# Kernel tuning notes

Hardware: AMD Instinct MI355X
Metric: run time of the kernel (lower is better)

## Reference

```python
import jax, jax.numpy as jnp
import numpy as np

EPS_LN = 1e-3
EPS_ATTN = 1e-8
D = 256       # slot_dim == feature_dim (required by the torch code)
H_MLP = 512
NUM_ITERS = 3  # step == 0 -> num_initial_iterations
SCALE = D ** (-0.5)


def _layernorm(x, g, b):
    m = jnp.mean(x, axis=-1, keepdims=True)
    v = jnp.mean(jnp.square(x - m), axis=-1, keepdims=True)
    return (x - m) * jax.lax.rsqrt(v + EPS_LN) * g + b


def _gru_cell(x, h, W_ih, b_ih, W_hh, b_hh):
    # torch GRUCell: W_ih [3D, D], W_hh [3D, D], gate order r, z, n
    gi = x @ W_ih.T + b_ih
    gh = h @ W_hh.T + b_hh
    i_r, i_z, i_n = jnp.split(gi, 3, axis=-1)
    h_r, h_z, h_n = jnp.split(gh, 3, axis=-1)
    r = jax.nn.sigmoid(i_r + h_r)
    z = jax.nn.sigmoid(i_z + h_z)
    n = jnp.tanh(i_n + r * h_n)
    return (1.0 - z) * n + z * h


def setup_inputs() -> dict:
    key = jax.random.key(0)
    ks = jax.random.split(key, 16)
    s = 0.02
    inp = {
        "inputs": jax.random.normal(ks[0], (32, 4096, D), jnp.float32),
        "slots": jax.random.normal(ks[1], (32, 8, D), jnp.float32),
        "step": 0,
        "ln_in_g": jnp.ones((D,), jnp.float32),
        "ln_in_b": jnp.zeros((D,), jnp.float32),
        "ln_slot_g": jnp.ones((D,), jnp.float32),
        "ln_slot_b": jnp.zeros((D,), jnp.float32),
        "ln_mlp_g": jnp.ones((D,), jnp.float32),
        "ln_mlp_b": jnp.zeros((D,), jnp.float32),
        "Wq": jax.random.normal(ks[2], (D, D), jnp.float32) * s,
        "bq": jnp.zeros((D,), jnp.float32),
        "Wk": jax.random.normal(ks[3], (D, D), jnp.float32) * s,
        "bk": jnp.zeros((D,), jnp.float32),
        "Wv": jax.random.normal(ks[4], (D, D), jnp.float32) * s,
        "bv": jnp.zeros((D,), jnp.float32),
        "W_ih": jax.random.normal(ks[5], (3 * D, D), jnp.float32) * s,
        "b_ih": jnp.zeros((3 * D,), jnp.float32),
        "W_hh": jax.random.normal(ks[6], (3 * D, D), jnp.float32) * s,
        "b_hh": jnp.zeros((3 * D,), jnp.float32),
        "W1": jax.random.normal(ks[7], (H_MLP, D), jnp.float32) * s,
        "b1": jnp.zeros((H_MLP,), jnp.float32),
        "W2": jax.random.normal(ks[8], (D, H_MLP), jnp.float32) * s,
        "b2": jnp.zeros((D,), jnp.float32),
    }
    return inp


def reference(inputs, slots, step, ln_in_g, ln_in_b, ln_slot_g, ln_slot_b,
              ln_mlp_g, ln_mlp_b, Wq, bq, Wk, bk, Wv, bv,
              W_ih, b_ih, W_hh, b_hh, W1, b1, W2, b2):
    B = inputs.shape[0]
    x = _layernorm(inputs, ln_in_g, ln_in_b)          # [B, N, D]
    k = x @ Wk.T + bk                                  # [B, N, D]
    v = x @ Wv.T + bv                                  # [B, N, D]
    num_iters = NUM_ITERS  # step == 0 -> num_initial_iterations
    for _ in range(num_iters):
        slots_prev = slots
        s_n = _layernorm(slots, ln_slot_g, ln_slot_b)  # [B, S, D]
        q = s_n @ Wq.T + bq                            # [B, S, D]
        dots = jnp.einsum('bid,bjd->bij', q, k) * SCALE  # [B, S, N]
        attn = jax.nn.softmax(dots, axis=1) + EPS_ATTN   # competitive over slots
        attn = attn / jnp.sum(attn, axis=-1, keepdims=True)
        updates = jnp.einsum('bij,bjd->bid', attn, v)  # [B, S, D]
        slots = _gru_cell(updates.reshape(-1, D), slots_prev.reshape(-1, D),
                          W_ih, b_ih, W_hh, b_hh).reshape(B, -1, D)
        mlp = jax.nn.relu(_layernorm(slots, ln_mlp_g, ln_mlp_b) @ W1.T + b1) @ W2.T + b2
        slots = slots + mlp
    return slots
```

## Files before the change

kernel.cpp:

```cpp
#include <hip/hip_runtime.h>
#include <stdint.h>


typedef __attribute__((ext_vector_type(8))) short bf16x8;
typedef __attribute__((ext_vector_type(4))) float f32x4;

__device__ __forceinline__ float bf2f_lo(uint32_t u) {
    union { uint32_t u; float f; } v; v.u = u << 16; return v.f;
}
__device__ __forceinline__ float bf2f_hi(uint32_t u) {
    union { uint32_t u; float f; } v; v.u = u & 0xffff0000u; return v.f;
}
__device__ __forceinline__ unsigned short f2bf(float f) {
    union { float f; uint32_t u; } v; v.f = f;
    return (unsigned short)((v.u + 0x7fffu + ((v.u >> 16) & 1u)) >> 16);
}
__device__ __forceinline__ void unpack8(uint4 v, float* f) {
    f[0] = bf2f_lo(v.x); f[1] = bf2f_hi(v.x); f[2] = bf2f_lo(v.y); f[3] = bf2f_hi(v.y);
    f[4] = bf2f_lo(v.z); f[5] = bf2f_hi(v.z); f[6] = bf2f_lo(v.w); f[7] = bf2f_hi(v.w);
}
__device__ __forceinline__ float sigf(float x) { return 1.0f / (1.0f + __expf(-x)); }
__device__ __forceinline__ void gld_lds16(const void* g, void* l) {
    __builtin_amdgcn_global_load_lds(
        (__attribute__((address_space(1))) unsigned int*)g,
        (__attribute__((address_space(3))) unsigned int*)l, 16, 0, 0);
}

__global__ __launch_bounds__(256) void prep_k(
    const float* __restrict__ in, const float* __restrict__ ln_in_g,
    const float* __restrict__ ln_in_b, unsigned short* __restrict__ xbf,
    const float* __restrict__ Wk, const float* __restrict__ Wv,
    const float* __restrict__ W_ih, const float* __restrict__ W_hh,
    const float* __restrict__ W1, const float* __restrict__ W2,
    const float* __restrict__ bk, const float* __restrict__ bv,
    const float* __restrict__ b_ih, const float* __restrict__ b_hh,
    unsigned short* __restrict__ Wkv, unsigned short* __restrict__ Wg,
    unsigned short* __restrict__ W1b, unsigned short* __restrict__ W2b,
    float* __restrict__ bkv, float* __restrict__ bg,
    const float* __restrict__ slots_in, const float* __restrict__ g_slot,
    const float* __restrict__ b_slot, const float* __restrict__ Wq,
    const float* __restrict__ bq, unsigned short* __restrict__ qbuf) {
    __shared__ __align__(16) unsigned short A1[8 * 264];
    int bid = blockIdx.x, t = threadIdx.x;
    int wave = t >> 6, lane = t & 63;

    if (bid < 32768) {
        size_t row = (size_t)bid * 4 + wave;
        const float4 x = *(const float4*)(in + row * 256 + lane * 4);
        float s  = x.x + x.y + x.z + x.w;
        float sq = x.x * x.x + x.y * x.y + x.z * x.z + x.w * x.w;
#pragma unroll
        for (int off = 32; off > 0; off >>= 1) {
            s  += __shfl_xor(s,  off, 64);
            sq += __shfl_xor(sq, off, 64);
        }
        float mean = s * (1.0f / 256.0f);
        float rstd = rsqrtf(sq * (1.0f / 256.0f) - mean * mean + 1e-3f);
        float4 g4 = *(const float4*)(ln_in_g + lane * 4);
        float4 b4 = *(const float4*)(ln_in_b + lane * 4);
        uint2 o;
        o.x = (uint32_t)f2bf((x.x - mean) * rstd * g4.x + b4.x) |
              ((uint32_t)f2bf((x.y - mean) * rstd * g4.y + b4.y) << 16);
        o.y = (uint32_t)f2bf((x.z - mean) * rstd * g4.z + b4.z) |
              ((uint32_t)f2bf((x.w - mean) * rstd * g4.w + b4.w) << 16);
        int dst = (((lane >> 1) ^ ((int)row & 7)) << 3) + (lane & 1) * 4;
        *(uint2*)(xbf + row * 256 + dst) = o;
        return;
    }
    if (bid < 36096) {
        int i = (bid - 32768) * 256 + t;
        if (i < 131072) {
            float v = (i < 65536) ? Wk[i] : Wv[i - 65536];
            int col = i >> 8, k = i & 255;
            int dk = ((((k >> 3) ^ (col & 7)) << 3) | (k & 7));
            Wkv[col * 256 + dk] = f2bf(v);
        } else if (i < 524288) {
            int j = i - 131072;
            Wg[j] = f2bf(j < 196608 ? W_ih[j] : W_hh[j - 196608]);
        } else if (i < 655360) W1b[i - 524288] = f2bf(W1[i - 524288]);
        else                   W2b[i - 655360] = f2bf(W2[i - 655360]);
        if (i < 512)           bkv[i] = (i < 256 ? bk[i] : bv[i - 256]);
        else if (i < 2048)   { int j = i - 512; bg[j] = (j < 768 ? b_ih[j] : b_hh[j - 768]); }
        return;
    }
    int b = bid - 36096;
    {
        float4 g4 = *(const float4*)(g_slot + lane * 4);
        float4 b4 = *(const float4*)(b_slot + lane * 4);
#pragma unroll
        for (int rep = 0; rep < 2; ++rep) {
            int s = wave * 2 + rep;
            float4 x = *(const float4*)(slots_in + (size_t)b * 2048 + s * 256 + lane * 4);
            float sm = x.x + x.y + x.z + x.w;
            float sq = x.x * x.x + x.y * x.y + x.z * x.z + x.w * x.w;
#pragma unroll
            for (int off = 32; off > 0; off >>= 1) {
                sm += __shfl_xor(sm, off, 64);
                sq += __shfl_xor(sq, off, 64);
            }
            float mean = sm * (1.0f / 256.0f);
            float rstd = rsqrtf(sq * (1.0f / 256.0f) - mean * mean + 1e-3f);
            uint2 o;
            o.x = (uint32_t)f2bf((x.x - mean) * rstd * g4.x + b4.x) |
                  ((uint32_t)f2bf((x.y - mean) * rstd * g4.y + b4.y) << 16);
            o.y = (uint32_t)f2bf((x.z - mean) * rstd * g4.z + b4.z) |
                  ((uint32_t)f2bf((x.w - mean) * rstd * g4.w + b4.w) << 16);
            *(uint2*)&A1[s * 264 + lane * 4] = o;
        }
    }
    __syncthreads();
    {
        bf16x8 af[8];
#pragma unroll
        for (int ks = 0; ks < 8; ++ks)
            af[ks] = *(const bf16x8*)&A1[(lane & 15) * 264 + ks * 32 + (lane >> 4) * 8];
#pragma unroll
        for (int nt = 0; nt < 4; ++nt) {
            int n0 = (wave * 4 + nt) * 16;
            f32x4 a = {0.f, 0.f, 0.f, 0.f};
#pragma unroll
            for (int ks = 0; ks < 8; ++ks) {
                const float* wp = Wq + (size_t)(n0 + (lane & 15)) * 256 +
                                  ks * 32 + (lane >> 4) * 8;
                float4 wa = *(const float4*)wp;
                float4 wb = *(const float4*)(wp + 4);
                bf16x8 bfr;
                bfr[0] = (short)f2bf(wa.x); bfr[1] = (short)f2bf(wa.y);
                bfr[2] = (short)f2bf(wa.z); bfr[3] = (short)f2bf(wa.w);
                bfr[4] = (short)f2bf(wb.x); bfr[5] = (short)f2bf(wb.y);
                bfr[6] = (short)f2bf(wb.z); bfr[7] = (short)f2bf(wb.w);
                a = __builtin_amdgcn_mfma_f32_16x16x32_bf16(af[ks], bfr, a, 0, 0, 0);
            }
            int col = n0 + (lane & 15);
            float bs = bq[col];
#pragma unroll
            for (int r = 0; r < 4; ++r) {
                int row = (lane >> 4) * 4 + r;
                if (row < 8)
                    qbuf[((size_t)b * 8 + row) * 256 + col] = f2bf(a[r] + bs);
            }
        }
    }
}

__global__ __launch_bounds__(256) void gemm_kv(const unsigned short* __restrict__ X,
                                               const unsigned short* __restrict__ W,
                                               const float* __restrict__ bkv,
                                               unsigned short* __restrict__ Ko,
                                               unsigned short* __restrict__ Vo) {
    __shared__ __align__(16) unsigned short As[128 * 64];
    __shared__ __align__(16) unsigned short Bs[128 * 64];
    int t = threadIdx.x, wave = t >> 6, lane = t & 63;
    int wr = wave >> 1, wc = wave & 1;
    int bid = blockIdx.x;
    int m0 = (((bid >> 5) << 3) | (bid & 7)) * 128;
    int j0 = ((bid >> 3) & 3) * 128;

    f32x4 acc[4][4];
#pragma unroll
    for (int i = 0; i < 4; ++i)
#pragma unroll
        for (int j = 0; j < 4; ++j)
#pragma unroll
            for (int r = 0; r < 4; ++r) acc[i][j][r] = 0.f;

    for (int kb = 0; kb < 4; ++kb) {
        int k0 = kb * 64;
#pragma unroll
        for (int i = 0; i < 4; ++i) {
            int rbase = wave * 32 + i * 8;
            gld_lds16(X + (size_t)(m0 + rbase + (lane >> 3)) * 256 + k0 + (lane & 7) * 8,
                      &As[rbase * 64]);
            gld_lds16(W + (size_t)(j0 + rbase + (lane >> 3)) * 256 + k0 + (lane & 7) * 8,
                      &Bs[rbase * 64]);
        }
        __syncthreads();
#pragma unroll
        for (int kk = 0; kk < 64; kk += 32) {
            int koff = kk + (lane >> 4) * 8;
            int cl = koff >> 3;
            bf16x8 af[4], bf[4];
#pragma unroll
            for (int ti = 0; ti < 4; ++ti) {
                int r = wr * 64 + ti * 16 + (lane & 15);
                af[ti] = *(const bf16x8*)&As[r * 64 + ((cl ^ (r & 7)) << 3)];
            }
#pragma unroll
            for (int tj = 0; tj < 4; ++tj) {
                int c = wc * 64 + tj * 16 + (lane & 15);
                bf[tj] = *(const bf16x8*)&Bs[c * 64 + ((cl ^ (c & 7)) << 3)];
            }
#pragma unroll
            for (int ti = 0; ti < 4; ++ti)
#pragma unroll
                for (int tj = 0; tj < 4; ++tj)
                    acc[ti][tj] = __builtin_amdgcn_mfma_f32_16x16x32_bf16(
                        af[ti], bf[tj], acc[ti][tj], 0, 0, 0);
        }
        __syncthreads();
    }
    bool isK = (j0 < 256);
    unsigned short* base = isK ? Ko : Vo;
#pragma unroll
    for (int ti = 0; ti < 4; ++ti)
#pragma unroll
        for (int tj = 0; tj < 4; ++tj) {
            int col = j0 + wc * 64 + tj * 16 + (lane & 15);
            float bias = bkv[col];
            int outc = col & 255;
#pragma unroll
            for (int r = 0; r < 4; ++r) {
                int row = m0 + wr * 64 + ti * 16 + (lane >> 4) * 4 + r;
                base[(size_t)row * 256 + outc] = f2bf(acc[ti][tj][r] + bias);
            }
        }
}

__global__ __launch_bounds__(256) void attn_fused(
    const unsigned short* __restrict__ qb, const unsigned short* __restrict__ K,
    const unsigned short* __restrict__ V,
    float* __restrict__ upd_p,
    float* __restrict__ sums_p) {
    __shared__ __align__(16) unsigned short qs[8 * 256];
    __shared__ __align__(16) float atf[8 * 256];
    __shared__ __align__(16) float pr[4][8 * 256];
    __shared__ float ssum[8];
    int b = blockIdx.x, ch = blockIdx.y, t = threadIdx.x;
    int wave = t >> 6, lane = t & 63;

    *(uint4*)&qs[t * 8] = ((const uint4*)(qb + b * 2048))[t];
    if (t < 8) ssum[t] = 0.f;
    __syncthreads();

    int sg = t >> 7, np = t & 127;
    int nbase = ch * 256 + np * 2;
    const unsigned short* kr = K + ((size_t)b * 4096 + nbase) * 256;
    float acc[4][2];
#pragma unroll
    for (int i = 0; i < 4; ++i) { acc[i][0] = 0.f; acc[i][1] = 0.f; }
    for (int c = 0; c < 32; ++c) {
        float qf[4][8];
#pragma unroll
        for (int si = 0; si < 4; ++si)
            unpack8(*(const uint4*)&qs[(sg * 4 + si) * 256 + c * 8], qf[si]);
#pragma unroll
        for (int r = 0; r < 2; ++r) {
            float kf[8];
            unpack8(*(const uint4*)(kr + (size_t)r * 256 + c * 8), kf);
#pragma unroll
            for (int si = 0; si < 4; ++si)
                acc[si][r] += qf[si][0] * kf[0] + qf[si][1] * kf[1] +
                              qf[si][2] * kf[2] + qf[si][3] * kf[3] +
                              qf[si][4] * kf[4] + qf[si][5] * kf[5] +
                              qf[si][6] * kf[6] + qf[si][7] * kf[7];
        }
    }
#pragma unroll
    for (int si = 0; si < 4; ++si) {
        atf[(sg * 4 + si) * 256 + np * 2 + 0] = acc[si][0] * 0.0625f;
        atf[(sg * 4 + si) * 256 + np * 2 + 1] = acc[si][1] * 0.0625f;
    }
    __syncthreads();

    {
        int n = t;
        float v[8];
#pragma unroll
        for (int s = 0; s < 8; ++s) v[s] = atf[s * 256 + n];
        float m = v[0];
#pragma unroll
        for (int s = 1; s < 8; ++s) m = fmaxf(m, v[s]);
        float sum = 0.f;
#pragma unroll
        for (int s = 0; s < 8; ++s) { v[s] = __expf(v[s] - m); sum += v[s]; }
        float inv = 1.0f / sum;
        float ts[8];
#pragma unroll
        for (int s = 0; s < 8; ++s) {
            float a = v[s] * inv + 1e-8f;
            atf[s * 256 + n] = a;
            ts[s] = a;
        }
#pragma unroll
        for (int s = 0; s < 8; ++s) {
#pragma unroll
            for (int off = 32; off > 0; off >>= 1)
                ts[s] += __shfl_xor(ts[s], off, 64);
        }
        if (lane == 0) {
#pragma unroll
            for (int s = 0; s < 8; ++s) atomicAdd(&ssum[s], ts[s]);
        }
    }
    __syncthreads();
    if (t < 8) sums_p[ch * 256 + b * 8 + t] = ssum[t];

    float ua[8][4];
#pragma unroll
    for (int s = 0; s < 8; ++s)
#pragma unroll
        for (int k = 0; k < 4; ++k) ua[s][k] = 0.f;
    const unsigned short* vb = V + ((size_t)b * 4096 + ch * 256 + wave * 64) * 256 + lane * 4;
    for (int g = 0; g < 16; ++g) {
        int nl = wave * 64 + g * 4;
        float4 a4[8];
#pragma unroll
        for (int s = 0; s < 8; ++s) a4[s] = *(const float4*)&atf[s * 256 + nl];
        const unsigned short* vrow = vb + (size_t)g * 4 * 256;
#define UPD_STEP(kk, comp)                                                     \
        {                                                                      \
            uint2 vv = *(const uint2*)(vrow + (size_t)kk * 256);               \
            float v0 = bf2f_lo(vv.x), v1 = bf2f_hi(vv.x);                      \
            float v2 = bf2f_lo(vv.y), v3 = bf2f_hi(vv.y);                      \
            _Pragma("unroll")                                                  \
            for (int s = 0; s < 8; ++s) {                                      \
                float a = a4[s].comp;                                          \
                ua[s][0] += a * v0; ua[s][1] += a * v1;                        \
                ua[s][2] += a * v2; ua[s][3] += a * v3;                        \
            }                                                                  \
        }
        UPD_STEP(0, x) UPD_STEP(1, y) UPD_STEP(2, z) UPD_STEP(3, w)
#undef UPD_STEP
    }
#pragma unroll
    for (int s = 0; s < 8; ++s)
        *(float4*)&pr[wave][s * 256 + lane * 4] = *(float4*)ua[s];
    __syncthreads();
    for (int i = t; i < 2048; i += 256)
        upd_p[(size_t)ch * 65536 + (size_t)b * 2048 + i] =
            pr[0][i] + pr[1][i] + pr[2][i] + pr[3][i];
}

__global__ __launch_bounds__(256) void slot_tail(
    const float* __restrict__ upd_p, const float* __restrict__ sums_p,
    const float* __restrict__ cur,
    const unsigned short* __restrict__ Wg, const float* __restrict__ bg,
    const float* __restrict__ g_mlp, const float* __restrict__ b_mlp,
    const unsigned short* __restrict__ W1b, const float* __restrict__ b1,
    const unsigned short* __restrict__ W2b, const float* __restrict__ b2,
    const float* __restrict__ g_slot, const float* __restrict__ b_slot,
    const unsigned short* __restrict__ Wqb, const float* __restrict__ bq,
    float* __restrict__ slots_out, unsigned short* __restrict__ qbuf,
    int do_q) {
    __shared__ float gts[8 * 1536];
    __shared__ float hn[2048];
    __shared__ float sn[2048];
    __shared__ __align__(16) unsigned short A1u[8 * 264];
    __shared__ __align__(16) unsigned short A1h[8 * 264];
    __shared__ __align__(16) unsigned short A1[8 * 264];
    __shared__ __align__(16) unsigned short A2[8 * 520];
    __shared__ float ssum8[8];
    int b = blockIdx.x, t = threadIdx.x;
    int wave = t >> 6, lane = t & 63;

    if (t < 8) {
        float s = 0.f;
#pragma unroll
        for (int c = 0; c < 16; ++c) s += sums_p[c * 256 + b * 8 + t];
        ssum8[t] = s;
    }
    __syncthreads();
    for (int idx = t; idx < 2048; idx += 256) {
        int row = idx >> 8, d = idx & 255;
        float us = 0.f;
#pragma unroll
        for (int c = 0; c < 16; ++c) us += upd_p[(size_t)c * 65536 + b * 2048 + idx];
        A1u[row * 264 + d] = f2bf(us / ssum8[row]);
        A1h[row * 264 + d] = f2bf(cur[(size_t)b * 2048 + idx]);
    }
    __syncthreads();

    {
        const unsigned short* Af = (wave < 2) ? A1u : A1h;
        bf16x8 af[8];
#pragma unroll
        for (int ks = 0; ks < 8; ++ks)
            af[ks] = *(const bf16x8*)&Af[(lane & 15) * 264 + ks * 32 + (lane >> 4) * 8];
#pragma unroll
        for (int nt = 0; nt < 24; ++nt) {
            int n0 = wave * 384 + nt * 16;
            f32x4 a = {0.f, 0.f, 0.f, 0.f};
#pragma unroll
            for (int ks = 0; ks < 8; ++ks) {
                bf16x8 bfr = *(const bf16x8*)(Wg + (size_t)(n0 + (lane & 15)) * 256 +
                                              ks * 32 + (lane >> 4) * 8);
                a = __builtin_amdgcn_mfma_f32_16x16x32_bf16(af[ks], bfr, a, 0, 0, 0);
            }
            int col = n0 + (lane & 15);
            float bs = bg[col];
#pragma unroll
            for (int r = 0; r < 4; ++r) {
                int row = (lane >> 4) * 4 + r;
                if (row < 8) gts[row * 1536 + col] = a[r] + bs;
            }
        }
    }
    __syncthreads();

#pragma unroll
    for (int p = 0; p < 8; ++p) {
        int idx = p * 256 + t;
        int s = idx >> 8, j = idx & 255;
        const float* gr = &gts[s * 1536];
        float r  = sigf(gr[j] + gr[768 + j]);
        float z  = sigf(gr[256 + j] + gr[1024 + j]);
        float nn = tanhf(gr[512 + j] + r * gr[1280 + j]);
        float h  = cur[(size_t)b * 2048 + idx];
        hn[idx] = (1.0f - z) * nn + z * h;
    }
    __syncthreads();

    {
        float4 g4 = *(const float4*)(g_mlp + lane * 4);
        float4 b4 = *(const float4*)(b_mlp + lane * 4);
#pragma unroll
        for (int rep = 0; rep < 2; ++rep) {
            int s = wave * 2 + rep;
            float4 x = *(const float4*)&hn[s * 256 + lane * 4];
            float sm = x.x + x.y + x.z + x.w;
            float sq = x.x * x.x + x.y * x.y + x.z * x.z + x.w * x.w;
#pragma unroll
            for (int off = 32; off > 0; off >>= 1) {
                sm += __shfl_xor(sm, off, 64);
                sq += __shfl_xor(sq, off, 64);
            }
            float mean = sm * (1.0f / 256.0f);
            float rstd = rsqrtf(sq * (1.0f / 256.0f) - mean * mean + 1e-3f);
            uint2 o;
            o.x = (uint32_t)f2bf((x.x - mean) * rstd * g4.x + b4.x) |
                  ((uint32_t)f2bf((x.y - mean) * rstd * g4.y + b4.y) << 16);
            o.y = (uint32_t)f2bf((x.z - mean) * rstd * g4.z + b4.z) |
                  ((uint32_t)f2bf((x.w - mean) * rstd * g4.w + b4.w) << 16);
            *(uint2*)&A1[s * 264 + lane * 4] = o;
        }
    }
    __syncthreads();

    {
        bf16x8 af[8];
#pragma unroll
        for (int ks = 0; ks < 8; ++ks)
            af[ks] = *(const bf16x8*)&A1[(lane & 15) * 264 + ks * 32 + (lane >> 4) * 8];
#pragma unroll
        for (int nt = 0; nt < 8; ++nt) {
            int n0 = (wave * 8 + nt) * 16;
            f32x4 a = {0.f, 0.f, 0.f, 0.f};
#pragma unroll
            for (int ks = 0; ks < 8; ++ks) {
                bf16x8 bfr = *(const bf16x8*)(W1b + (size_t)(n0 + (lane & 15)) * 256 +
                                              ks * 32 + (lane >> 4) * 8);
                a = __builtin_amdgcn_mfma_f32_16x16x32_bf16(af[ks], bfr, a, 0, 0, 0);
            }
            int col = n0 + (lane & 15);
            float bs = b1[col];
#pragma unroll
            for (int r = 0; r < 4; ++r) {
                int row = (lane >> 4) * 4 + r;
                if (row < 8) A2[row * 520 + col] = f2bf(fmaxf(a[r] + bs, 0.f));
            }
        }
    }
    __syncthreads();

    {
        bf16x8 af[16];
#pragma unroll
        for (int ks = 0; ks < 16; ++ks)
            af[ks] = *(const bf16x8*)&A2[(lane & 15) * 520 + ks * 32 + (lane >> 4) * 8];
#pragma unroll
        for (int nt = 0; nt < 4; ++nt) {
            int n0 = (wave * 4 + nt) * 16;
            f32x4 a = {0.f, 0.f, 0.f, 0.f};
#pragma unroll
            for (int ks = 0; ks < 16; ++ks) {
                bf16x8 bfr = *(const bf16x8*)(W2b + (size_t)(n0 + (lane & 15)) * 512 +
                                              ks * 32 + (lane >> 4) * 8);
                a = __builtin_amdgcn_mfma_f32_16x16x32_bf16(af[ks], bfr, a, 0, 0, 0);
            }
            int col = n0 + (lane & 15);
            float bs = b2[col];
#pragma unroll
            for (int r = 0; r < 4; ++r) {
                int row = (lane >> 4) * 4 + r;
                if (row < 8) {
                    float v = a[r] + bs + hn[row * 256 + col];
                    sn[row * 256 + col] = v;
                    slots_out[((size_t)b * 8 + row) * 256 + col] = v;
                }
            }
        }
    }
    if (!do_q) return;
    __syncthreads();

    {
        float4 g4 = *(const float4*)(g_slot + lane * 4);
        float4 b4 = *(const float4*)(b_slot + lane * 4);
#pragma unroll
        for (int rep = 0; rep < 2; ++rep) {
            int s = wave * 2 + rep;
            float4 x = *(const float4*)&sn[s * 256 + lane * 4];
            float sm = x.x + x.y + x.z + x.w;
            float sq = x.x * x.x + x.y * x.y + x.z * x.z + x.w * x.w;
#pragma unroll
            for (int off = 32; off > 0; off >>= 1) {
                sm += __shfl_xor(sm, off, 64);
                sq += __shfl_xor(sq, off, 64);
            }
            float mean = sm * (1.0f / 256.0f);
            float rstd = rsqrtf(sq * (1.0f / 256.0f) - mean * mean + 1e-3f);
            uint2 o;
            o.x = (uint32_t)f2bf((x.x - mean) * rstd * g4.x + b4.x) |
                  ((uint32_t)f2bf((x.y - mean) * rstd * g4.y + b4.y) << 16);
            o.y = (uint32_t)f2bf((x.z - mean) * rstd * g4.z + b4.z) |
                  ((uint32_t)f2bf((x.w - mean) * rstd * g4.w + b4.w) << 16);
            *(uint2*)&A1[s * 264 + lane * 4] = o;
        }
    }
    __syncthreads();

    {
        bf16x8 af[8];
#pragma unroll
        for (int ks = 0; ks < 8; ++ks)
            af[ks] = *(const bf16x8*)&A1[(lane & 15) * 264 + ks * 32 + (lane >> 4) * 8];
#pragma unroll
        for (int nt = 0; nt < 4; ++nt) {
            int n0 = (wave * 4 + nt) * 16;
            f32x4 a = {0.f, 0.f, 0.f, 0.f};
#pragma unroll
            for (int ks = 0; ks < 8; ++ks) {
                bf16x8 bfr = *(const bf16x8*)(Wqb + (size_t)(n0 + (lane & 15)) * 256 +
                                              ks * 32 + (lane >> 4) * 8);
                a = __builtin_amdgcn_mfma_f32_16x16x32_bf16(af[ks], bfr, a, 0, 0, 0);
            }
            int col = n0 + (lane & 15);
            float bs = bq[col];
#pragma unroll
            for (int r = 0; r < 4; ++r) {
                int row = (lane >> 4) * 4 + r;
                if (row < 8)
                    qbuf[((size_t)b * 8 + row) * 256 + col] = f2bf(a[r] + bs);
            }
        }
    }
}

extern "C" void kernel_launch(void* const* d_in, const int* in_sizes, int n_in,
                              void* d_out, int out_size, void* d_ws, size_t ws_size,
                              hipStream_t stream) {
    const float* inputs    = (const float*)d_in[0];
    const float* slots_in  = (const float*)d_in[1];
    const float* ln_in_g   = (const float*)d_in[3];
    const float* ln_in_b   = (const float*)d_in[4];
    const float* ln_slot_g = (const float*)d_in[5];
    const float* ln_slot_b = (const float*)d_in[6];
    const float* ln_mlp_g  = (const float*)d_in[7];
    const float* ln_mlp_b  = (const float*)d_in[8];
    const float* Wq   = (const float*)d_in[9];
    const float* bq   = (const float*)d_in[10];
    const float* Wk   = (const float*)d_in[11];
    const float* bk   = (const float*)d_in[12];
    const float* Wv   = (const float*)d_in[13];
    const float* bv   = (const float*)d_in[14];
    const float* W_ih = (const float*)d_in[15];
    const float* b_ih = (const float*)d_in[16];
    const float* W_hh = (const float*)d_in[17];
    const float* b_hh = (const float*)d_in[18];
    const float* W1   = (const float*)d_in[19];
    const float* b1   = (const float*)d_in[20];
    const float* W2   = (const float*)d_in[21];
    const float* b2   = (const float*)d_in[22];

    char* p = (char*)d_ws;
    size_t off = 0;
    auto take = [&](size_t bytes) -> char* {
        char* r = p + off;
        off += (bytes + 255) & ~(size_t)255;
        return r;
    };
    unsigned short* xbf  = (unsigned short*)take((size_t)131072 * 256 * 2);
    unsigned short* Kb   = (unsigned short*)take((size_t)131072 * 256 * 2);
    unsigned short* Vb   = (unsigned short*)take((size_t)131072 * 256 * 2);
    unsigned short* Wkv  = (unsigned short*)take(131072 * 2);
    unsigned short* Wg   = (unsigned short*)take(393216 * 2);
    unsigned short* W1b  = (unsigned short*)take(131072 * 2);
    unsigned short* W2b  = (unsigned short*)take(131072 * 2);
    unsigned short* Wqb  = (unsigned short*)take(65536 * 2);
    float* bkv   = (float*)take(512 * 4);
    float* bg    = (float*)take(1536 * 4);
    unsigned short* qbuf = (unsigned short*)take(65536 * 2);
    float* upd_p = (float*)take((size_t)16 * 65536 * 4);
    float* sums_p= (float*)take(16 * 256 * 4);
    float* sA    = (float*)take(65536 * 4);
    float* sB    = (float*)take(65536 * 4);


    prep_k<<<36128, 256, 0, stream>>>(inputs, ln_in_g, ln_in_b, xbf,
                                      Wk, Wv, W_ih, W_hh, W1, W2,
                                      bk, bv, b_ih, b_hh,
                                      Wkv, Wg, W1b, W2b, bkv, bg,
                                      slots_in, ln_slot_g, ln_slot_b, Wq, bq, qbuf);
    {
        struct L { static __global__ void k(const float* __restrict__ Wq,
                                            unsigned short* __restrict__ Wqb) {
            int i = blockIdx.x * 256 + threadIdx.x;
            Wqb[i] = f2bf(Wq[i]);
        } };
        L::k<<<256, 256, 0, stream>>>(Wq, Wqb);
    }
    gemm_kv<<<4096, 256, 0, stream>>>(xbf, Wkv, bkv, Kb, Vb);

    const float* cur = slots_in;
    float* nxt[3] = {sA, sB, (float*)d_out};
    for (int it = 0; it < 3; ++it) {
        attn_fused<<<dim3(32, 16), 256, 0, stream>>>(qbuf, Kb, Vb, upd_p, sums_p);
        slot_tail<<<32, 256, 0, stream>>>(upd_p, sums_p, cur, Wg, bg,
                                          ln_mlp_g, ln_mlp_b, W1b, b1, W2b, b2,
                                          ln_slot_g, ln_slot_b, Wqb, bq,
                                          nxt[it], qbuf, it < 2 ? 1 : 0);
        cur = nxt[it];
    }
    (void)in_sizes; (void)n_in; (void)out_size; (void)ws_size;
}
```

Before: 618.2 us.

## Accumulate attention partials with atomics and widen slot_tail to 512 threads

```diff
diff --git a/kernel.cpp b/kernel.cpp
--- a/kernel.cpp
+++ b/kernel.cpp
@@ -39,36 +39,52 @@
     float* __restrict__ bkv, float* __restrict__ bg,
     const float* __restrict__ slots_in, const float* __restrict__ g_slot,
     const float* __restrict__ b_slot, const float* __restrict__ Wq,
-    const float* __restrict__ bq, unsigned short* __restrict__ qbuf) {
+    const float* __restrict__ bq, unsigned short* __restrict__ qbuf,
+    float* __restrict__ upd) {
     __shared__ __align__(16) unsigned short A1[8 * 264];
     int bid = blockIdx.x, t = threadIdx.x;
     int wave = t >> 6, lane = t & 63;
 
-    if (bid < 32768) {
-        size_t row = (size_t)bid * 4 + wave;
-        const float4 x = *(const float4*)(in + row * 256 + lane * 4);
-        float s  = x.x + x.y + x.z + x.w;
-        float sq = x.x * x.x + x.y * x.y + x.z * x.z + x.w * x.w;
+    if (bid < 8192) {
+        size_t rb = (size_t)bid * 16 + wave * 4;
+        const float* rp = in + rb * 256 + lane * 4;
+        float4 x0 = *(const float4*)(rp);
+        float4 x1 = *(const float4*)(rp + 256);
+        float4 x2 = *(const float4*)(rp + 512);
+        float4 x3 = *(const float4*)(rp + 768);
+        float s0 = x0.x + x0.y + x0.z + x0.w, q0 = x0.x*x0.x + x0.y*x0.y + x0.z*x0.z + x0.w*x0.w;
+        float s1 = x1.x + x1.y + x1.z + x1.w, q1 = x1.x*x1.x + x1.y*x1.y + x1.z*x1.z + x1.w*x1.w;
+        float s2 = x2.x + x2.y + x2.z + x2.w, q2 = x2.x*x2.x + x2.y*x2.y + x2.z*x2.z + x2.w*x2.w;
+        float s3 = x3.x + x3.y + x3.z + x3.w, q3 = x3.x*x3.x + x3.y*x3.y + x3.z*x3.z + x3.w*x3.w;
 #pragma unroll
         for (int off = 32; off > 0; off >>= 1) {
-            s  += __shfl_xor(s,  off, 64);
-            sq += __shfl_xor(sq, off, 64);
-        }
-        float mean = s * (1.0f / 256.0f);
-        float rstd = rsqrtf(sq * (1.0f / 256.0f) - mean * mean + 1e-3f);
+            s0 += __shfl_xor(s0, off, 64);  q0 += __shfl_xor(q0, off, 64);
+            s1 += __shfl_xor(s1, off, 64);  q1 += __shfl_xor(q1, off, 64);
+            s2 += __shfl_xor(s2, off, 64);  q2 += __shfl_xor(q2, off, 64);
+            s3 += __shfl_xor(s3, off, 64);  q3 += __shfl_xor(q3, off, 64);
+        }
         float4 g4 = *(const float4*)(ln_in_g + lane * 4);
         float4 b4 = *(const float4*)(ln_in_b + lane * 4);
-        uint2 o;
-        o.x = (uint32_t)f2bf((x.x - mean) * rstd * g4.x + b4.x) |
-              ((uint32_t)f2bf((x.y - mean) * rstd * g4.y + b4.y) << 16);
-        o.y = (uint32_t)f2bf((x.z - mean) * rstd * g4.z + b4.z) |
-              ((uint32_t)f2bf((x.w - mean) * rstd * g4.w + b4.w) << 16);
-        int dst = (((lane >> 1) ^ ((int)row & 7)) << 3) + (lane & 1) * 4;
-        *(uint2*)(xbf + row * 256 + dst) = o;
+        float4 xs[4] = {x0, x1, x2, x3};
+        float ss[4] = {s0, s1, s2, s3}, qq[4] = {q0, q1, q2, q3};
+#pragma unroll
+        for (int i = 0; i < 4; ++i) {
+            float mean = ss[i] * (1.0f / 256.0f);
+            float rstd = rsqrtf(qq[i] * (1.0f / 256.0f) - mean * mean + 1e-3f);
+            float4 x = xs[i];
+            uint2 o;
+            o.x = (uint32_t)f2bf((x.x - mean) * rstd * g4.x + b4.x) |
+                  ((uint32_t)f2bf((x.y - mean) * rstd * g4.y + b4.y) << 16);
+            o.y = (uint32_t)f2bf((x.z - mean) * rstd * g4.z + b4.z) |
+                  ((uint32_t)f2bf((x.w - mean) * rstd * g4.w + b4.w) << 16);
+            size_t row = rb + i;
+            int dst = (((lane >> 1) ^ ((int)row & 7)) << 3) + (lane & 1) * 4;
+            *(uint2*)(xbf + row * 256 + dst) = o;
+        }
         return;
     }
-    if (bid < 36096) {
-        int i = (bid - 32768) * 256 + t;
+    if (bid < 11520) {
+        int i = (bid - 8192) * 256 + t;
         if (i < 131072) {
             float v = (i < 65536) ? Wk[i] : Wv[i - 65536];
             int col = i >> 8, k = i & 255;
@@ -83,7 +99,12 @@
         else if (i < 2048)   { int j = i - 512; bg[j] = (j < 768 ? b_ih[j] : b_hh[j - 768]); }
         return;
     }
-    int b = bid - 36096;
+    if (bid >= 11552) {
+        int i = (bid - 11552) * 1024 + t * 4;
+        if (i < 65792) *(float4*)(upd + i) = make_float4(0.f, 0.f, 0.f, 0.f);
+        return;
+    }
+    int b = bid - 11520;
     {
         float4 g4 = *(const float4*)(g_slot + lane * 4);
         float4 b4 = *(const float4*)(b_slot + lane * 4);
@@ -219,8 +240,7 @@
 __global__ __launch_bounds__(256) void attn_fused(
     const unsigned short* __restrict__ qb, const unsigned short* __restrict__ K,
     const unsigned short* __restrict__ V,
-    float* __restrict__ upd_p,
-    float* __restrict__ sums_p) {
+    float* __restrict__ upd, float* __restrict__ sums) {
     __shared__ __align__(16) unsigned short qs[8 * 256];
     __shared__ __align__(16) float atf[8 * 256];
     __shared__ __align__(16) float pr[4][8 * 256];
@@ -293,7 +313,7 @@
         }
     }
     __syncthreads();
-    if (t < 8) sums_p[ch * 256 + b * 8 + t] = ssum[t];
+    if (t < 8) atomicAdd(&sums[b * 8 + t], ssum[t]);
 
     float ua[8][4];
 #pragma unroll
@@ -326,13 +346,15 @@
     for (int s = 0; s < 8; ++s)
         *(float4*)&pr[wave][s * 256 + lane * 4] = *(float4*)ua[s];
     __syncthreads();
-    for (int i = t; i < 2048; i += 256)
-        upd_p[(size_t)ch * 65536 + (size_t)b * 2048 + i] =
-            pr[0][i] + pr[1][i] + pr[2][i] + pr[3][i];
-}
-
-__global__ __launch_bounds__(256) void slot_tail(
-    const float* __restrict__ upd_p, const float* __restrict__ sums_p,
+    for (int i = t; i < 2048; i += 256) {
+        float vsum = pr[0][i] + pr[1][i] + pr[2][i] + pr[3][i];
+        atomicAdd(&upd[(size_t)b * 2048 + i], vsum);
+    }
+}
+
+__global__ __launch_bounds__(512, 1) void slot_tail(
+    const float* __restrict__ upd, const float* __restrict__ sums,
+    float* __restrict__ upd_w, float* __restrict__ sums_w,
     const float* __restrict__ cur,
     const unsigned short* __restrict__ Wg, const float* __restrict__ bg,
     const float* __restrict__ g_mlp, const float* __restrict__ b_mlp,
@@ -353,32 +375,26 @@
     int b = blockIdx.x, t = threadIdx.x;
     int wave = t >> 6, lane = t & 63;
 
-    if (t < 8) {
-        float s = 0.f;
-#pragma unroll
-        for (int c = 0; c < 16; ++c) s += sums_p[c * 256 + b * 8 + t];
-        ssum8[t] = s;
-    }
-    __syncthreads();
-    for (int idx = t; idx < 2048; idx += 256) {
+    if (t < 8) ssum8[t] = sums[b * 8 + t];
+    __syncthreads();
+    for (int idx = t; idx < 2048; idx += 512) {
         int row = idx >> 8, d = idx & 255;
-        float us = 0.f;
-#pragma unroll
-        for (int c = 0; c < 16; ++c) us += upd_p[(size_t)c * 65536 + b * 2048 + idx];
-        A1u[row * 264 + d] = f2bf(us / ssum8[row]);
+        A1u[row * 264 + d] = f2bf(upd[(size_t)b * 2048 + idx] / ssum8[row]);
         A1h[row * 264 + d] = f2bf(cur[(size_t)b * 2048 + idx]);
     }
     __syncthreads();
-
-    {
-        const unsigned short* Af = (wave < 2) ? A1u : A1h;
+    for (int idx = t; idx < 2048; idx += 512) upd_w[(size_t)b * 2048 + idx] = 0.f;
+    if (t < 8) sums_w[b * 8 + t] = 0.f;
+
+    {
+        const unsigned short* Af = (wave < 4) ? A1u : A1h;
         bf16x8 af[8];
 #pragma unroll
         for (int ks = 0; ks < 8; ++ks)
             af[ks] = *(const bf16x8*)&Af[(lane & 15) * 264 + ks * 32 + (lane >> 4) * 8];
 #pragma unroll
-        for (int nt = 0; nt < 24; ++nt) {
-            int n0 = wave * 384 + nt * 16;
+        for (int nt = 0; nt < 12; ++nt) {
+            int n0 = wave * 192 + nt * 16;
             f32x4 a = {0.f, 0.f, 0.f, 0.f};
 #pragma unroll
             for (int ks = 0; ks < 8; ++ks) {
@@ -398,8 +414,8 @@
     __syncthreads();
 
 #pragma unroll
-    for (int p = 0; p < 8; ++p) {
-        int idx = p * 256 + t;
+    for (int p = 0; p < 4; ++p) {
+        int idx = p * 512 + t;
         int s = idx >> 8, j = idx & 255;
         const float* gr = &gts[s * 1536];
         float r  = sigf(gr[j] + gr[768 + j]);
@@ -413,26 +429,23 @@
     {
         float4 g4 = *(const float4*)(g_mlp + lane * 4);
         float4 b4 = *(const float4*)(b_mlp + lane * 4);
-#pragma unroll
-        for (int rep = 0; rep < 2; ++rep) {
-            int s = wave * 2 + rep;
-            float4 x = *(const float4*)&hn[s * 256 + lane * 4];
-            float sm = x.x + x.y + x.z + x.w;
-            float sq = x.x * x.x + x.y * x.y + x.z * x.z + x.w * x.w;
-#pragma unroll
-            for (int off = 32; off > 0; off >>= 1) {
-                sm += __shfl_xor(sm, off, 64);
-                sq += __shfl_xor(sq, off, 64);
-            }
-            float mean = sm * (1.0f / 256.0f);
-            float rstd = rsqrtf(sq * (1.0f / 256.0f) - mean * mean + 1e-3f);
-            uint2 o;
-            o.x = (uint32_t)f2bf((x.x - mean) * rstd * g4.x + b4.x) |
-                  ((uint32_t)f2bf((x.y - mean) * rstd * g4.y + b4.y) << 16);
-            o.y = (uint32_t)f2bf((x.z - mean) * rstd * g4.z + b4.z) |
-                  ((uint32_t)f2bf((x.w - mean) * rstd * g4.w + b4.w) << 16);
-            *(uint2*)&A1[s * 264 + lane * 4] = o;
-        }
+        int s = wave;
+        float4 x = *(const float4*)&hn[s * 256 + lane * 4];
+        float sm = x.x + x.y + x.z + x.w;
+        float sq = x.x * x.x + x.y * x.y + x.z * x.z + x.w * x.w;
+#pragma unroll
+        for (int off = 32; off > 0; off >>= 1) {
+            sm += __shfl_xor(sm, off, 64);
+            sq += __shfl_xor(sq, off, 64);
+        }
+        float mean = sm * (1.0f / 256.0f);
+        float rstd = rsqrtf(sq * (1.0f / 256.0f) - mean * mean + 1e-3f);
+        uint2 o;
+        o.x = (uint32_t)f2bf((x.x - mean) * rstd * g4.x + b4.x) |
+              ((uint32_t)f2bf((x.y - mean) * rstd * g4.y + b4.y) << 16);
+        o.y = (uint32_t)f2bf((x.z - mean) * rstd * g4.z + b4.z) |
+              ((uint32_t)f2bf((x.w - mean) * rstd * g4.w + b4.w) << 16);
+        *(uint2*)&A1[s * 264 + lane * 4] = o;
     }
     __syncthreads();
 
@@ -442,8 +455,8 @@
         for (int ks = 0; ks < 8; ++ks)
             af[ks] = *(const bf16x8*)&A1[(lane & 15) * 264 + ks * 32 + (lane >> 4) * 8];
 #pragma unroll
-        for (int nt = 0; nt < 8; ++nt) {
-            int n0 = (wave * 8 + nt) * 16;
+        for (int nt = 0; nt < 4; ++nt) {
+            int n0 = (wave * 4 + nt) * 16;
             f32x4 a = {0.f, 0.f, 0.f, 0.f};
 #pragma unroll
             for (int ks = 0; ks < 8; ++ks) {
@@ -468,8 +481,8 @@
         for (int ks = 0; ks < 16; ++ks)
             af[ks] = *(const bf16x8*)&A2[(lane & 15) * 520 + ks * 32 + (lane >> 4) * 8];
 #pragma unroll
-        for (int nt = 0; nt < 4; ++nt) {
-            int n0 = (wave * 4 + nt) * 16;
+        for (int nt = 0; nt < 2; ++nt) {
+            int n0 = (wave * 2 + nt) * 16;
             f32x4 a = {0.f, 0.f, 0.f, 0.f};
 #pragma unroll
             for (int ks = 0; ks < 16; ++ks) {
@@ -496,26 +509,23 @@
     {
         float4 g4 = *(const float4*)(g_slot + lane * 4);
         float4 b4 = *(const float4*)(b_slot + lane * 4);
-#pragma unroll
-        for (int rep = 0; rep < 2; ++rep) {
-            int s = wave * 2 + rep;
-            float4 x = *(const float4*)&sn[s * 256 + lane * 4];
-            float sm = x.x + x.y + x.z + x.w;
-            float sq = x.x * x.x + x.y * x.y + x.z * x.z + x.w * x.w;
-#pragma unroll
-            for (int off = 32; off > 0; off >>= 1) {
-                sm += __shfl_xor(sm, off, 64);
-                sq += __shfl_xor(sq, off, 64);
-            }
-            float mean = sm * (1.0f / 256.0f);
-            float rstd = rsqrtf(sq * (1.0f / 256.0f) - mean * mean + 1e-3f);
-            uint2 o;
-            o.x = (uint32_t)f2bf((x.x - mean) * rstd * g4.x + b4.x) |
-                  ((uint32_t)f2bf((x.y - mean) * rstd * g4.y + b4.y) << 16);
-            o.y = (uint32_t)f2bf((x.z - mean) * rstd * g4.z + b4.z) |
-                  ((uint32_t)f2bf((x.w - mean) * rstd * g4.w + b4.w) << 16);
-            *(uint2*)&A1[s * 264 + lane * 4] = o;
-        }
+        int s = wave;
+        float4 x = *(const float4*)&sn[s * 256 + lane * 4];
+        float sm = x.x + x.y + x.z + x.w;
+        float sq = x.x * x.x + x.y * x.y + x.z * x.z + x.w * x.w;
+#pragma unroll
+        for (int off = 32; off > 0; off >>= 1) {
+            sm += __shfl_xor(sm, off, 64);
+            sq += __shfl_xor(sq, off, 64);
+        }
+        float mean = sm * (1.0f / 256.0f);
+        float rstd = rsqrtf(sq * (1.0f / 256.0f) - mean * mean + 1e-3f);
+        uint2 o;
+        o.x = (uint32_t)f2bf((x.x - mean) * rstd * g4.x + b4.x) |
+              ((uint32_t)f2bf((x.y - mean) * rstd * g4.y + b4.y) << 16);
+        o.y = (uint32_t)f2bf((x.z - mean) * rstd * g4.z + b4.z) |
+              ((uint32_t)f2bf((x.w - mean) * rstd * g4.w + b4.w) << 16);
+        *(uint2*)&A1[s * 264 + lane * 4] = o;
     }
     __syncthreads();
 
@@ -525,8 +535,8 @@
         for (int ks = 0; ks < 8; ++ks)
             af[ks] = *(const bf16x8*)&A1[(lane & 15) * 264 + ks * 32 + (lane >> 4) * 8];
 #pragma unroll
-        for (int nt = 0; nt < 4; ++nt) {
-            int n0 = (wave * 4 + nt) * 16;
+        for (int nt = 0; nt < 2; ++nt) {
+            int n0 = (wave * 2 + nt) * 16;
             f32x4 a = {0.f, 0.f, 0.f, 0.f};
 #pragma unroll
             for (int ks = 0; ks < 8; ++ks) {
@@ -590,17 +600,17 @@
     float* bkv   = (float*)take(512 * 4);
     float* bg    = (float*)take(1536 * 4);
     unsigned short* qbuf = (unsigned short*)take(65536 * 2);
-    float* upd_p = (float*)take((size_t)16 * 65536 * 4);
-    float* sums_p= (float*)take(16 * 256 * 4);
+    float* upd   = (float*)take((65536 + 256) * 4);
+    float* sums  = upd + 65536;
     float* sA    = (float*)take(65536 * 4);
     float* sB    = (float*)take(65536 * 4);
 
-
-    prep_k<<<36128, 256, 0, stream>>>(inputs, ln_in_g, ln_in_b, xbf,
+    prep_k<<<11617, 256, 0, stream>>>(inputs, ln_in_g, ln_in_b, xbf,
                                       Wk, Wv, W_ih, W_hh, W1, W2,
                                       bk, bv, b_ih, b_hh,
                                       Wkv, Wg, W1b, W2b, bkv, bg,
-                                      slots_in, ln_slot_g, ln_slot_b, Wq, bq, qbuf);
+                                      slots_in, ln_slot_g, ln_slot_b, Wq, bq, qbuf,
+                                      upd);
     {
         struct L { static __global__ void k(const float* __restrict__ Wq,
                                             unsigned short* __restrict__ Wqb) {
@@ -614,8 +624,8 @@
     const float* cur = slots_in;
     float* nxt[3] = {sA, sB, (float*)d_out};
     for (int it = 0; it < 3; ++it) {
-        attn_fused<<<dim3(32, 16), 256, 0, stream>>>(qbuf, Kb, Vb, upd_p, sums_p);
-        slot_tail<<<32, 256, 0, stream>>>(upd_p, sums_p, cur, Wg, bg,
+        attn_fused<<<dim3(32, 16), 256, 0, stream>>>(qbuf, Kb, Vb, upd, sums);
+        slot_tail<<<32, 512, 0, stream>>>(upd, sums, upd, sums, cur, Wg, bg,
                                           ln_mlp_g, ln_mlp_b, W1b, b1, W2b, b2,
                                           ln_slot_g, ln_slot_b, Wqb, bq,
                                           nxt[it], qbuf, it < 2 ? 1 : 0);
```

Result: faster. 558.6 us (-9.6%).
